# Performance work log

Measured on AMD Instinct MI355X. Metric: run time of the kernel, lower is better.

## Reference

```python
import jax, jax.numpy as jnp
import numpy as np
from jax import lax

B, T, D, LD, K = 128, 1024, 256, 512, 128
RD = LD + K  # 640 residual-LSTM width
PAD = 15     # (31 - 1) // 2 'same' padding for the LSA location conv


def _gru(x, h, wih, whh, bih, bhh):
    # torch.nn.GRUCell semantics, gate order [r, z, n]
    gi = x @ wih.T + bih
    gh = h @ whh.T + bhh
    ir, iz, inn = jnp.split(gi, 3, axis=-1)
    hr, hz, hn = jnp.split(gh, 3, axis=-1)
    r = jax.nn.sigmoid(ir + hr)
    z = jax.nn.sigmoid(iz + hz)
    n = jnp.tanh(inn + r * hn)
    return (1.0 - z) * n + z * h


def _lstm(x, h, c, wih, whh, bih, bhh):
    # torch.nn.LSTMCell semantics, gate order [i, f, g, o]
    g = x @ wih.T + bih + h @ whh.T + bhh
    i, f, gg, o = jnp.split(g, 4, axis=-1)
    c2 = jax.nn.sigmoid(f) * c + jax.nn.sigmoid(i) * jnp.tanh(gg)
    h2 = jax.nn.sigmoid(o) * jnp.tanh(c2)
    return h2, c2


def _forward(encoder_seq, encoder_seq_proj, prenet_in, attn_hidden, rnn1_h, rnn1_c,
             rnn2_h, rnn2_c, res_h, res_c, context_vec, cumulative, attn_prev,
             fc1_w, fc1_b, fc2_w, fc2_b, gru_wih, gru_whh, gru_bih, gru_bhh,
             conv_w, L_w, L_b, W_w, W_b, v_w, ri_w, ri_b,
             r1_wih, r1_whh, r1_bih, r1_bhh, r2_wih, r2_whh, r2_bih, r2_bhh,
             res_wih, res_whh, res_bih, res_bhh, stop_w, stop_b):
    # PreNet (dropout p = 0 in Decoder.__init__, so pure tanh-MLP)
    p = jnp.tanh(prenet_in @ fc1_w.T + fc1_b)
    prenet_out = jnp.tanh(p @ fc2_w.T + fc2_b)                     # [B, D//2]
    # Attention GRU
    attn_in = jnp.concatenate([context_vec, prenet_out], axis=-1)  # [B, D + D//2]
    attn_h = _gru(attn_in, attn_hidden, gru_wih, gru_whh, gru_bih, gru_bhh)  # [B, D]
    # LSA location-sensitive attention (cumulative/attn_prev are zeros at t=0)
    pq = (attn_h @ W_w.T + W_b)[:, None, :]                        # [B, 1, D]
    loc = jnp.stack([cumulative, attn_prev], axis=1)               # [B, 2, T]
    conv_out = lax.conv_general_dilated(loc, conv_w, (1,), [(PAD, PAD)],
                                        dimension_numbers=('NCH', 'OIH', 'NCH'))  # [B, 32, T]
    ploc = jnp.swapaxes(conv_out, 1, 2) @ L_w.T + L_b              # [B, T, D]
    u = jnp.squeeze(jnp.tanh(pq + encoder_seq_proj + ploc) @ v_w.T, -1)  # [B, T]
    sig = jax.nn.sigmoid(u)
    scores = sig / jnp.sum(sig, axis=1, keepdims=True)             # [B, T]
    cum_new = cumulative + scores
    context = jnp.einsum('bt,btd->bd', scores, encoder_seq)        # [B, D]
    # rnn_input projection + two residual LSTM cells (eval: no zoneout)
    x = jnp.concatenate([context, attn_h], axis=1) @ ri_w.T + ri_b  # [B, LD]
    h1, c1 = _lstm(x, rnn1_h, rnn1_c, r1_wih, r1_whh, r1_bih, r1_bhh)
    x = x + h1
    h2, c2 = _lstm(x, rnn2_h, rnn2_c, r2_wih, r2_whh, r2_bih, r2_bhh)
    x = x + h2
    # 4-layer residual LSTM stack on [prenet_in, x]
    res_x = jnp.concatenate([prenet_in, x], axis=1)                # [B, RD]
    hs, cs = [], []
    for i in range(4):
        hi, ci = _lstm(res_x, res_h[i], res_c[i], res_wih[i], res_whh[i], res_bih[i], res_bhh[i])
        res_x = res_x + hi
        hs.append(hi)
        cs.append(ci)
    cond = res_x                                                   # cond_features [B, RD]
    stop = jax.nn.sigmoid(cond @ stop_w.T + stop_b)                # [B, 1]
    return (cond, stop, scores, attn_h, h1, c1, h2, c2,
            jnp.stack(hs), jnp.stack(cs), context, cum_new)


def setup_inputs() -> dict:
    keys = iter(jax.random.split(jax.random.key(0), 64))
    nxt = lambda: next(keys)
    rn = lambda s: jax.random.normal(nxt(), s, jnp.float32)
    wp = lambda s: rn(s) * 0.02
    return {
        'encoder_seq': rn((B, T, D)),
        'encoder_seq_proj': rn((B, T, D)),
        'prenet_in': rn((B, K)),
        'attn_hidden': rn((B, D)),
        'rnn1_h': rn((B, LD)), 'rnn1_c': rn((B, LD)),
        'rnn2_h': rn((B, LD)), 'rnn2_c': rn((B, LD)),
        'res_h': rn((4, B, RD)), 'res_c': rn((4, B, RD)),
        'context_vec': rn((B, D)),
        'cumulative': jnp.zeros((B, T), jnp.float32),
        'attn_prev': jnp.zeros((B, T), jnp.float32),
        'fc1_w': wp((256, K)), 'fc1_b': jnp.zeros((256,), jnp.float32),
        'fc2_w': wp((D // 2, 256)), 'fc2_b': jnp.zeros((D // 2,), jnp.float32),
        'gru_wih': wp((3 * D, D + D // 2)), 'gru_whh': wp((3 * D, D)),
        'gru_bih': jnp.zeros((3 * D,), jnp.float32), 'gru_bhh': jnp.zeros((3 * D,), jnp.float32),
        'conv_w': wp((32, 2, 31)),
        'L_w': wp((D, 32)), 'L_b': jnp.zeros((D,), jnp.float32),
        'W_w': wp((D, D)), 'W_b': jnp.zeros((D,), jnp.float32),
        'v_w': wp((1, D)),
        'ri_w': wp((LD, 2 * D)), 'ri_b': jnp.zeros((LD,), jnp.float32),
        'r1_wih': wp((4 * LD, LD)), 'r1_whh': wp((4 * LD, LD)),
        'r1_bih': jnp.zeros((4 * LD,), jnp.float32), 'r1_bhh': jnp.zeros((4 * LD,), jnp.float32),
        'r2_wih': wp((4 * LD, LD)), 'r2_whh': wp((4 * LD, LD)),
        'r2_bih': jnp.zeros((4 * LD,), jnp.float32), 'r2_bhh': jnp.zeros((4 * LD,), jnp.float32),
        'res_wih': wp((4, 4 * RD, RD)), 'res_whh': wp((4, 4 * RD, RD)),
        'res_bih': jnp.zeros((4, 4 * RD), jnp.float32), 'res_bhh': jnp.zeros((4, 4 * RD), jnp.float32),
        'stop_w': wp((1, RD)), 'stop_b': jnp.zeros((1,), jnp.float32),
    }


def reference(encoder_seq, encoder_seq_proj, prenet_in, attn_hidden, rnn1_h, rnn1_c,
              rnn2_h, rnn2_c, res_h, res_c, context_vec, cumulative, attn_prev,
              fc1_w, fc1_b, fc2_w, fc2_b, gru_wih, gru_whh, gru_bih, gru_bhh,
              conv_w, L_w, L_b, W_w, W_b, v_w, ri_w, ri_b,
              r1_wih, r1_whh, r1_bih, r1_bhh, r2_wih, r2_whh, r2_bih, r2_bhh,
              res_wih, res_whh, res_bih, res_bhh, stop_w, stop_b):
    return _forward(encoder_seq, encoder_seq_proj, prenet_in, attn_hidden, rnn1_h, rnn1_c,
                    rnn2_h, rnn2_c, res_h, res_c, context_vec, cumulative, attn_prev,
                    fc1_w, fc1_b, fc2_w, fc2_b, gru_wih, gru_whh, gru_bih, gru_bhh,
                    conv_w, L_w, L_b, W_w, W_b, v_w, ri_w, ri_b,
                    r1_wih, r1_whh, r1_bih, r1_bhh, r2_wih, r2_whh, r2_bih, r2_bhh,
                    res_wih, res_whh, res_bih, res_bhh, stop_w, stop_b)
```

## Files before the change

### kernel.cpp

```cpp
#include <hip/hip_runtime.h>

#define DEV __device__ __forceinline__

DEV float sigm(float x) { return 1.0f / (1.0f + __expf(-x)); }
DEV float tanhf_fast(float x) { return 1.0f - 2.0f / (1.0f + __expf(2.0f * x)); }

__global__ __launch_bounds__(256) void gemm2s_kernel(
    const float* __restrict__ A1, int K1, const float* __restrict__ W1, int ldw1,
    const float* __restrict__ A2, int K2, const float* __restrict__ W2, int ldw2,
    float* __restrict__ Cp, int N, int KS, int KC)
{
    __shared__ float As[16][128];
    __shared__ float Ws[16][33];
    const int tid = threadIdx.x;
    const int chunk = blockIdx.x % KS;
    const int n0 = (blockIdx.x / KS) * 32;
    const int kbeg = chunk * KC;
    const int kend = kbeg + KC;
    const int tx = tid & 15, ty = tid >> 4;
    const int lm = tid & 127, lk = (tid >> 7) * 8;

    float acc[16];
#pragma unroll
    for (int i = 0; i < 16; ++i) acc[i] = 0.f;

    for (int k0 = kbeg; k0 < kend; k0 += 16) {
        const float* A; const float* W; int lda, ldw, kc;
        if (k0 < K1) { A = A1; W = W1; lda = K1; ldw = ldw1; kc = k0; }
        else         { A = A2; W = W2; lda = K2; ldw = ldw2; kc = k0 - K1; }

        float4 a0 = *(const float4*)(A + (size_t)lm * lda + kc + lk);
        float4 a1 = *(const float4*)(A + (size_t)lm * lda + kc + lk + 4);
        As[lk + 0][lm] = a0.x; As[lk + 1][lm] = a0.y;
        As[lk + 2][lm] = a0.z; As[lk + 3][lm] = a0.w;
        As[lk + 4][lm] = a1.x; As[lk + 5][lm] = a1.y;
        As[lk + 6][lm] = a1.z; As[lk + 7][lm] = a1.w;
        if (tid < 128) {
            int nl = tid >> 2, kq = (tid & 3) * 4;
            float4 w = *(const float4*)(W + (size_t)(n0 + nl) * ldw + kc + kq);
            Ws[kq + 0][nl] = w.x; Ws[kq + 1][nl] = w.y;
            Ws[kq + 2][nl] = w.z; Ws[kq + 3][nl] = w.w;
        }
        __syncthreads();
#pragma unroll
        for (int kk = 0; kk < 16; ++kk) {
            float w0 = Ws[kk][tx * 2 + 0];
            float w1 = Ws[kk][tx * 2 + 1];
            float4 x0 = *(const float4*)&As[kk][ty * 8];
            float4 x1 = *(const float4*)&As[kk][ty * 8 + 4];
            acc[0] += x0.x * w0; acc[1] += x0.y * w0;
            acc[2] += x0.z * w0; acc[3] += x0.w * w0;
            acc[4] += x1.x * w0; acc[5] += x1.y * w0;
            acc[6] += x1.z * w0; acc[7] += x1.w * w0;
            acc[8]  += x0.x * w1; acc[9]  += x0.y * w1;
            acc[10] += x0.z * w1; acc[11] += x0.w * w1;
            acc[12] += x1.x * w1; acc[13] += x1.y * w1;
            acc[14] += x1.z * w1; acc[15] += x1.w * w1;
        }
        __syncthreads();
    }

    float* Co = Cp + (size_t)chunk * 128 * N;
#pragma unroll
    for (int j = 0; j < 2; ++j) {
        int n = n0 + tx * 2 + j;
#pragma unroll
        for (int i = 0; i < 8; ++i)
            Co[(size_t)(ty * 8 + i) * N + n] = acc[j * 8 + i];
    }
}

__global__ void reduce_act_kernel(const float* __restrict__ p, int KS, int MN,
                                  const float* __restrict__ b,
                                  float* __restrict__ out, int N, int act)
{
    int idx = blockIdx.x * 256 + threadIdx.x;
    if (idx >= MN) return;
    int n = idx % N;
    float v = b ? b[n] : 0.f;
    for (int s = 0; s < KS; ++s) v += p[(size_t)s * MN + idx];
    if (act) v = tanhf_fast(v);
    out[idx] = v;
}

__global__ void gru_gate_kernel(const float* __restrict__ gi_p, int KSi,
                                const float* __restrict__ gh_p, int KSh,
                                const float* __restrict__ bih, const float* __restrict__ bhh,
                                const float* __restrict__ h, float* __restrict__ out)
{
    const size_t MN = 128 * 768;
    int m = blockIdx.x, d = threadIdx.x;
    size_t base = (size_t)m * 768 + d;
    float ir = bih[d], iz = bih[256 + d], in = bih[512 + d];
    for (int s = 0; s < KSi; ++s) {
        const float* p = gi_p + s * MN + base;
        ir += p[0]; iz += p[256]; in += p[512];
    }
    float hr = bhh[d], hz = bhh[256 + d], hn = bhh[512 + d];
    for (int s = 0; s < KSh; ++s) {
        const float* p = gh_p + s * MN + base;
        hr += p[0]; hz += p[256]; hn += p[512];
    }
    float r = sigm(ir + hr);
    float z = sigm(iz + hz);
    float n = tanhf_fast(in + r * hn);
    out[m * 256 + d] = (1.f - z) * n + z * h[m * 256 + d];
}

__global__ void lstm_gate_kernel(const float* __restrict__ gp, int KS,
                                 const float* __restrict__ bih, const float* __restrict__ bhh,
                                 const float* __restrict__ c_in,
                                 float* __restrict__ h_out, float* __restrict__ c_out,
                                 float* __restrict__ xacc, int H)
{
    int d = blockIdx.x * 256 + threadIdx.x;
    int m = blockIdx.y;
    if (d >= H) return;
    const size_t MN = (size_t)128 * 4 * H;
    size_t base = (size_t)m * 4 * H + d;
    float iv = bih[d] + bhh[d];
    float fv = bih[H + d] + bhh[H + d];
    float gv = bih[2 * H + d] + bhh[2 * H + d];
    float ov = bih[3 * H + d] + bhh[3 * H + d];
    for (int s = 0; s < KS; ++s) {
        const float* p = gp + s * MN + base;
        iv += p[0]; fv += p[H]; gv += p[2 * H]; ov += p[3 * H];
    }
    float c2 = sigm(fv) * c_in[m * H + d] + sigm(iv) * tanhf_fast(gv);
    float h2 = sigm(ov) * tanhf_fast(c2);
    h_out[m * H + d] = h2;
    c_out[m * H + d] = c2;
    if (xacc) xacc[m * H + d] += h2;
}

__global__ void transpose_lw_kernel(const float* __restrict__ Lw, float* __restrict__ LwT)
{
    int i = blockIdx.x * 256 + threadIdx.x;
    int c = i >> 8, d = i & 255;
    LwT[i] = Lw[d * 32 + c];
}

__global__ __launch_bounds__(256) void attn_u_kernel(
    const float* __restrict__ esp, const float* __restrict__ pq,
    const float* __restrict__ LwT, const float* __restrict__ Lb,
    const float* __restrict__ vw, const float* __restrict__ cw,
    const float* __restrict__ cum, const float* __restrict__ prev,
    float* __restrict__ sig_out)
{
    const int b = blockIdx.x >> 4;
    const int t0 = (blockIdx.x & 15) << 6;
    const int tid = threadIdx.x;

    __shared__ float cum_s[96], prev_s[96];
    __shared__ float cw_s[2][32][33];
    __shared__ float conv_s[32][68];
    __shared__ float Lw_s[32][256];
    __shared__ float pq_s[256], vw_s[256];

    if (tid < 94) {
        int ti = t0 - 15 + tid;
        cum_s[tid] = (ti >= 0 && ti < 1024) ? cum[b * 1024 + ti] : 0.f;
    } else if (tid >= 128 && tid < 222) {
        int i = tid - 128;
        int ti = t0 - 15 + i;
        prev_s[i] = (ti >= 0 && ti < 1024) ? prev[b * 1024 + ti] : 0.f;
    }
    for (int i = tid; i < 2048; i += 256) {
        int which = i >> 10, c = (i >> 5) & 31, k = i & 31;
        cw_s[which][c][k] = (k < 31) ? cw[(c * 2 + which) * 31 + k] : 0.f;
    }
    for (int i = tid; i < 8192; i += 256)
        (&Lw_s[0][0])[i] = LwT[i];
    pq_s[tid] = pq[b * 256 + tid] + Lb[tid];
    vw_s[tid] = vw[tid];
    __syncthreads();

    {
        int c = tid & 31, t8 = (tid >> 5) << 3;
        float a[8] = {0.f, 0.f, 0.f, 0.f, 0.f, 0.f, 0.f, 0.f};
        for (int k = 0; k < 31; ++k) {
            float w0 = cw_s[0][c][k], w1 = cw_s[1][c][k];
#pragma unroll
            for (int j = 0; j < 8; ++j)
                a[j] += w0 * cum_s[t8 + j + k] + w1 * prev_s[t8 + j + k];
        }
#pragma unroll
        for (int j = 0; j < 8; ++j) conv_s[c][t8 + j] = a[j];
    }
    __syncthreads();

    const int dg = (tid & 31) << 3;
    const int tg = (tid >> 5) << 3;
    float pl[8][8] = {};
#pragma unroll 4
    for (int c = 0; c < 32; ++c) {
        float4 lw0 = *(const float4*)&Lw_s[c][dg];
        float4 lw1 = *(const float4*)&Lw_s[c][dg + 4];
        float4 cv0 = *(const float4*)&conv_s[c][tg];
        float4 cv1 = *(const float4*)&conv_s[c][tg + 4];
        float lwv[8] = {lw0.x, lw0.y, lw0.z, lw0.w, lw1.x, lw1.y, lw1.z, lw1.w};
        float cvv[8] = {cv0.x, cv0.y, cv0.z, cv0.w, cv1.x, cv1.y, cv1.z, cv1.w};
#pragma unroll
        for (int jt = 0; jt < 8; ++jt)
#pragma unroll
            for (int jd = 0; jd < 8; ++jd)
                pl[jt][jd] += cvv[jt] * lwv[jd];
    }

    float4 pa = *(const float4*)&pq_s[dg];
    float4 pb = *(const float4*)&pq_s[dg + 4];
    float4 va = *(const float4*)&vw_s[dg];
    float4 vb = *(const float4*)&vw_s[dg + 4];
    float pqv[8] = {pa.x, pa.y, pa.z, pa.w, pb.x, pb.y, pb.z, pb.w};
    float vwv[8] = {va.x, va.y, va.z, va.w, vb.x, vb.y, vb.z, vb.w};

    float part[8];
#pragma unroll
    for (int jt = 0; jt < 8; ++jt) {
        int t = t0 + tg + jt;
        const float* er = esp + ((long)(b * 1024 + t) << 8) + dg;
        float4 e0 = *(const float4*)er;
        float4 e1 = *(const float4*)(er + 4);
        float ev[8] = {e0.x, e0.y, e0.z, e0.w, e1.x, e1.y, e1.z, e1.w};
        float s = 0.f;
#pragma unroll
        for (int jd = 0; jd < 8; ++jd)
            s += tanhf_fast(pqv[jd] + ev[jd] + pl[jt][jd]) * vwv[jd];
        part[jt] = s;
    }
#pragma unroll
    for (int off = 1; off < 32; off <<= 1)
#pragma unroll
        for (int jt = 0; jt < 8; ++jt)
            part[jt] += __shfl_xor(part[jt], off);
    if ((tid & 31) == 0) {
#pragma unroll
        for (int jt = 0; jt < 8; ++jt)
            sig_out[b * 1024 + t0 + tg + jt] = sigm(part[jt]);
    }
}

__global__ void attn_norm_kernel(const float* __restrict__ sig, const float* __restrict__ cum,
                                 float* __restrict__ scores, float* __restrict__ cum_new,
                                 float* __restrict__ ctx)
{
    __shared__ float red[4];
    int b = blockIdx.x, tid = threadIdx.x;
    float4 sv = *(const float4*)&sig[b * 1024 + tid * 4];
    float s = sv.x + sv.y + sv.z + sv.w;
#pragma unroll
    for (int off = 1; off < 64; off <<= 1) s += __shfl_xor(s, off);
    if ((tid & 63) == 0) red[tid >> 6] = s;
    __syncthreads();
    float inv = 1.f / (red[0] + red[1] + red[2] + red[3]);
    float4 cv = *(const float4*)&cum[b * 1024 + tid * 4];
    float4 sc = {sv.x * inv, sv.y * inv, sv.z * inv, sv.w * inv};
    *(float4*)&scores[b * 1024 + tid * 4] = sc;
    float4 cn = {cv.x + sc.x, cv.y + sc.y, cv.z + sc.z, cv.w + sc.w};
    *(float4*)&cum_new[b * 1024 + tid * 4] = cn;
    ctx[b * 256 + tid] = 0.f;
}

__global__ void attn_ctx_kernel(const float* __restrict__ scores, const float* __restrict__ es,
                                float* __restrict__ ctx)
{
    __shared__ float sc_s[256];
    int b = blockIdx.x >> 2;
    int tbase = (blockIdx.x & 3) * 256;
    int tid = threadIdx.x;
    sc_s[tid] = scores[b * 1024 + tbase + tid];
    __syncthreads();
    float a = 0.f;
    const float* ep = es + ((size_t)(b * 1024 + tbase)) * 256 + tid;
#pragma unroll 4
    for (int tt = 0; tt < 256; ++tt)
        a += sc_s[tt] * ep[(size_t)tt * 256];
    atomicAdd(&ctx[b * 256 + tid], a);
}

__global__ void build_rescat_kernel(const float* __restrict__ pre, const float* __restrict__ x,
                                    float* __restrict__ res)
{
    int idx = blockIdx.x * 256 + threadIdx.x;
    int m = idx / 640, d = idx - m * 640;
    res[idx] = (d < 128) ? pre[m * 128 + d] : x[m * 512 + d - 128];
}

__global__ void copy_kernel(const float* __restrict__ src, float* __restrict__ dst, int n)
{
    int idx = blockIdx.x * 256 + threadIdx.x;
    if (idx < n) dst[idx] = src[idx];
}

__global__ void stop_kernel(const float* __restrict__ res, const float* __restrict__ sw,
                            const float* __restrict__ sb, float* __restrict__ stop)
{
    int m = blockIdx.x, lane = threadIdx.x;
    float s = 0.f;
    for (int k = lane; k < 640; k += 64) s += res[m * 640 + k] * sw[k];
#pragma unroll
    for (int off = 1; off < 64; off <<= 1) s += __shfl_xor(s, off);
    if (lane == 0) stop[m] = sigm(s + sb[0]);
}

extern "C" void kernel_launch(void* const* d_in, const int* in_sizes, int n_in,
                              void* d_out, int out_size, void* d_ws, size_t ws_size,
                              hipStream_t stream)
{
    const float* encoder_seq      = (const float*)d_in[0];
    const float* encoder_seq_proj = (const float*)d_in[1];
    const float* prenet_in        = (const float*)d_in[2];
    const float* attn_hidden      = (const float*)d_in[3];
    const float* rnn1_h  = (const float*)d_in[4];
    const float* rnn1_c  = (const float*)d_in[5];
    const float* rnn2_h  = (const float*)d_in[6];
    const float* rnn2_c  = (const float*)d_in[7];
    const float* res_h   = (const float*)d_in[8];
    const float* res_c   = (const float*)d_in[9];
    const float* context_vec = (const float*)d_in[10];
    const float* cumulative  = (const float*)d_in[11];
    const float* attn_prev   = (const float*)d_in[12];
    const float* fc1_w = (const float*)d_in[13];
    const float* fc1_b = (const float*)d_in[14];
    const float* fc2_w = (const float*)d_in[15];
    const float* fc2_b = (const float*)d_in[16];
    const float* gru_wih = (const float*)d_in[17];
    const float* gru_whh = (const float*)d_in[18];
    const float* gru_bih = (const float*)d_in[19];
    const float* gru_bhh = (const float*)d_in[20];
    const float* conv_w = (const float*)d_in[21];
    const float* L_w = (const float*)d_in[22];
    const float* L_b = (const float*)d_in[23];
    const float* W_w = (const float*)d_in[24];
    const float* W_b = (const float*)d_in[25];
    const float* v_w = (const float*)d_in[26];
    const float* ri_w = (const float*)d_in[27];
    const float* ri_b = (const float*)d_in[28];
    const float* r1_wih = (const float*)d_in[29];
    const float* r1_whh = (const float*)d_in[30];
    const float* r1_bih = (const float*)d_in[31];
    const float* r1_bhh = (const float*)d_in[32];
    const float* r2_wih = (const float*)d_in[33];
    const float* r2_whh = (const float*)d_in[34];
    const float* r2_bih = (const float*)d_in[35];
    const float* r2_bhh = (const float*)d_in[36];
    const float* res_wih = (const float*)d_in[37];
    const float* res_whh = (const float*)d_in[38];
    const float* res_bih = (const float*)d_in[39];
    const float* res_bhh = (const float*)d_in[40];
    const float* stop_w = (const float*)d_in[41];
    const float* stop_b = (const float*)d_in[42];

    float* ws  = (float*)d_ws;
    float* out = (float*)d_out;

    const size_t OFF_P    = 0;
    const size_t OFF_POUT = 32768;
    const size_t OFF_PQ   = 49152;
    const size_t OFF_SIG  = 81920;
    const size_t OFF_X    = 212992;
    const size_t OFF_RES  = 278528;
    const size_t OFF_LWT  = 360448;
    const size_t OFF_PART = 368640;
    const size_t OFF_PARTB = OFF_PART + (size_t)8 * 128 * 768;

    const size_t O_COND   = 0;
    const size_t O_STOP   = 81920;
    const size_t O_SCORES = 82048;
    const size_t O_ATTNH  = 213120;
    const size_t O_H1     = 245888;
    const size_t O_C1     = 311424;
    const size_t O_H2     = 376960;
    const size_t O_C2     = 442496;
    const size_t O_HS     = 508032;
    const size_t O_CS     = 835712;
    const size_t O_CTX    = 1163392;
    const size_t O_CUM    = 1196160;

    transpose_lw_kernel<<<32, 256, 0, stream>>>(L_w, ws + OFF_LWT);

    gemm2s_kernel<<<8 * 4, 256, 0, stream>>>(prenet_in, 128, fc1_w, 128,
                                             nullptr, 0, nullptr, 0,
                                             ws + OFF_PART, 256, 4, 32);
    reduce_act_kernel<<<128, 256, 0, stream>>>(ws + OFF_PART, 4, 128 * 256, fc1_b,
                                               ws + OFF_P, 256, 1);
    gemm2s_kernel<<<4 * 8, 256, 0, stream>>>(ws + OFF_P, 256, fc2_w, 256,
                                             nullptr, 0, nullptr, 0,
                                             ws + OFF_PART, 128, 8, 32);
    reduce_act_kernel<<<64, 256, 0, stream>>>(ws + OFF_PART, 8, 128 * 128, fc2_b,
                                              ws + OFF_POUT, 128, 1);

    gemm2s_kernel<<<24 * 8, 256, 0, stream>>>(context_vec, 256, gru_wih, 384,
                                              ws + OFF_POUT, 128, gru_wih + 256, 384,
                                              ws + OFF_PART, 768, 8, 48);
    gemm2s_kernel<<<24 * 8, 256, 0, stream>>>(attn_hidden, 256, gru_whh, 256,
                                              nullptr, 0, nullptr, 0,
                                              ws + OFF_PARTB, 768, 8, 32);
    gru_gate_kernel<<<128, 256, 0, stream>>>(ws + OFF_PART, 8, ws + OFF_PARTB, 8,
                                             gru_bih, gru_bhh, attn_hidden, out + O_ATTNH);

    gemm2s_kernel<<<8 * 8, 256, 0, stream>>>(out + O_ATTNH, 256, W_w, 256,
                                             nullptr, 0, nullptr, 0,
                                             ws + OFF_PART, 256, 8, 32);
    reduce_act_kernel<<<128, 256, 0, stream>>>(ws + OFF_PART, 8, 128 * 256, W_b,
                                               ws + OFF_PQ, 256, 0);

    attn_u_kernel<<<2048, 256, 0, stream>>>(encoder_seq_proj, ws + OFF_PQ, ws + OFF_LWT,
                                            L_b, v_w, conv_w, cumulative, attn_prev,
                                            ws + OFF_SIG);
    attn_norm_kernel<<<128, 256, 0, stream>>>(ws + OFF_SIG, cumulative,
                                              out + O_SCORES, out + O_CUM, out + O_CTX);
    attn_ctx_kernel<<<512, 256, 0, stream>>>(out + O_SCORES, encoder_seq, out + O_CTX);

    gemm2s_kernel<<<16 * 8, 256, 0, stream>>>(out + O_CTX, 256, ri_w, 512,
                                              out + O_ATTNH, 256, ri_w + 256, 512,
                                              ws + OFF_PART, 512, 8, 64);
    reduce_act_kernel<<<256, 256, 0, stream>>>(ws + OFF_PART, 8, 128 * 512, ri_b,
                                               ws + OFF_X, 512, 0);

    gemm2s_kernel<<<64 * 8, 256, 0, stream>>>(ws + OFF_X, 512, r1_wih, 512,
                                              rnn1_h, 512, r1_whh, 512,
                                              ws + OFF_PART, 2048, 8, 128);
    lstm_gate_kernel<<<dim3(2, 128), 256, 0, stream>>>(ws + OFF_PART, 8, r1_bih, r1_bhh,
                                                       rnn1_c, out + O_H1, out + O_C1,
                                                       ws + OFF_X, 512);
    gemm2s_kernel<<<64 * 8, 256, 0, stream>>>(ws + OFF_X, 512, r2_wih, 512,
                                              rnn2_h, 512, r2_whh, 512,
                                              ws + OFF_PART, 2048, 8, 128);
    lstm_gate_kernel<<<dim3(2, 128), 256, 0, stream>>>(ws + OFF_PART, 8, r2_bih, r2_bhh,
                                                       rnn2_c, out + O_H2, out + O_C2,
                                                       ws + OFF_X, 512);

    build_rescat_kernel<<<320, 256, 0, stream>>>(prenet_in, ws + OFF_X, ws + OFF_RES);

    for (int i = 0; i < 4; ++i) {
        const float* wih = res_wih + (size_t)i * 2560 * 640;
        const float* whh = res_whh + (size_t)i * 2560 * 640;
        gemm2s_kernel<<<80 * 8, 256, 0, stream>>>(ws + OFF_RES, 640, wih, 640,
                                                  res_h + (size_t)i * 81920, 640, whh, 640,
                                                  ws + OFF_PART, 2560, 8, 160);
        lstm_gate_kernel<<<dim3(3, 128), 256, 0, stream>>>(ws + OFF_PART, 8,
                                                           res_bih + (size_t)i * 2560,
                                                           res_bhh + (size_t)i * 2560,
                                                           res_c + (size_t)i * 81920,
                                                           out + O_HS + (size_t)i * 81920,
                                                           out + O_CS + (size_t)i * 81920,
                                                           ws + OFF_RES, 640);
    }

    copy_kernel<<<320, 256, 0, stream>>>(ws + OFF_RES, out + O_COND, 128 * 640);
    stop_kernel<<<128, 64, 0, stream>>>(ws + OFF_RES, stop_w, stop_b, out + O_STOP);
}
```

Baseline: 672.4 us.

## Use bf16 MFMA for location projection, double-buffer GEMM, split context kernel

The location-feature projection inside the attention-energy kernel now runs as a bf16 16x16x32 MFMA. The conv output and L_w are rounded to bf16 in shared memory, replacing the fp32 outer-product loop. The split-K GEMM gains register-staged double buffering so global loads for the next tile overlap compute on the current one. The context kernel is split into twice as many blocks over shorter time chunks, and sigmoid/tanh/normalisation use hardware reciprocal. The bf16 rounding and approximate reciprocal reduce precision.

```diff
diff --git a/kernel.cpp b/kernel.cpp
--- a/kernel.cpp
+++ b/kernel.cpp
@@ -2,21 +2,31 @@
 
 #define DEV __device__ __forceinline__
 
-DEV float sigm(float x) { return 1.0f / (1.0f + __expf(-x)); }
-DEV float tanhf_fast(float x) { return 1.0f - 2.0f / (1.0f + __expf(2.0f * x)); }
+typedef __attribute__((ext_vector_type(8))) short short8;
+typedef __attribute__((ext_vector_type(4))) float f32x4;
+
+DEV float fast_rcp(float x) { return __builtin_amdgcn_rcpf(x); }
+DEV float sigm(float x) { return fast_rcp(1.0f + __expf(-x)); }
+DEV float tanhf_fast(float x) { return 1.0f - 2.0f * fast_rcp(1.0f + __expf(2.0f * x)); }
+
+DEV short f2bf(float f) {
+    unsigned u = __float_as_uint(f);
+    unsigned r = (u + 0x7FFFu + ((u >> 16) & 1u)) >> 16;
+    return (short)r;
+}
 
 __global__ __launch_bounds__(256) void gemm2s_kernel(
     const float* __restrict__ A1, int K1, const float* __restrict__ W1, int ldw1,
     const float* __restrict__ A2, int K2, const float* __restrict__ W2, int ldw2,
     float* __restrict__ Cp, int N, int KS, int KC)
 {
-    __shared__ float As[16][128];
-    __shared__ float Ws[16][33];
+    __shared__ float As[2][16][128];
+    __shared__ float Ws[2][16][33];
     const int tid = threadIdx.x;
     const int chunk = blockIdx.x % KS;
     const int n0 = (blockIdx.x / KS) * 32;
     const int kbeg = chunk * KC;
-    const int kend = kbeg + KC;
+    const int nt = KC / 16;
     const int tx = tid & 15, ty = tid >> 4;
     const int lm = tid & 127, lk = (tid >> 7) * 8;
 
@@ -24,30 +34,43 @@
 #pragma unroll
     for (int i = 0; i < 16; ++i) acc[i] = 0.f;
 
-    for (int k0 = kbeg; k0 < kend; k0 += 16) {
+    float4 ra0, ra1, rw;
+    auto load_regs = [&](int k0) {
         const float* A; const float* W; int lda, ldw, kc;
         if (k0 < K1) { A = A1; W = W1; lda = K1; ldw = ldw1; kc = k0; }
         else         { A = A2; W = W2; lda = K2; ldw = ldw2; kc = k0 - K1; }
-
-        float4 a0 = *(const float4*)(A + (size_t)lm * lda + kc + lk);
-        float4 a1 = *(const float4*)(A + (size_t)lm * lda + kc + lk + 4);
-        As[lk + 0][lm] = a0.x; As[lk + 1][lm] = a0.y;
-        As[lk + 2][lm] = a0.z; As[lk + 3][lm] = a0.w;
-        As[lk + 4][lm] = a1.x; As[lk + 5][lm] = a1.y;
-        As[lk + 6][lm] = a1.z; As[lk + 7][lm] = a1.w;
+        ra0 = *(const float4*)(A + (size_t)lm * lda + kc + lk);
+        ra1 = *(const float4*)(A + (size_t)lm * lda + kc + lk + 4);
         if (tid < 128) {
             int nl = tid >> 2, kq = (tid & 3) * 4;
-            float4 w = *(const float4*)(W + (size_t)(n0 + nl) * ldw + kc + kq);
-            Ws[kq + 0][nl] = w.x; Ws[kq + 1][nl] = w.y;
-            Ws[kq + 2][nl] = w.z; Ws[kq + 3][nl] = w.w;
+            rw = *(const float4*)(W + (size_t)(n0 + nl) * ldw + kc + kq);
         }
-        __syncthreads();
+    };
+    auto store_lds = [&](int buf) {
+        As[buf][lk + 0][lm] = ra0.x; As[buf][lk + 1][lm] = ra0.y;
+        As[buf][lk + 2][lm] = ra0.z; As[buf][lk + 3][lm] = ra0.w;
+        As[buf][lk + 4][lm] = ra1.x; As[buf][lk + 5][lm] = ra1.y;
+        As[buf][lk + 6][lm] = ra1.z; As[buf][lk + 7][lm] = ra1.w;
+        if (tid < 128) {
+            int nl = tid >> 2, kq = (tid & 3) * 4;
+            Ws[buf][kq + 0][nl] = rw.x; Ws[buf][kq + 1][nl] = rw.y;
+            Ws[buf][kq + 2][nl] = rw.z; Ws[buf][kq + 3][nl] = rw.w;
+        }
+    };
+
+    load_regs(kbeg);
+    store_lds(0);
+    __syncthreads();
+
+    for (int it = 0; it < nt; ++it) {
+        const int cur = it & 1;
+        if (it + 1 < nt) load_regs(kbeg + (it + 1) * 16);
 #pragma unroll
         for (int kk = 0; kk < 16; ++kk) {
-            float w0 = Ws[kk][tx * 2 + 0];
-            float w1 = Ws[kk][tx * 2 + 1];
-            float4 x0 = *(const float4*)&As[kk][ty * 8];
-            float4 x1 = *(const float4*)&As[kk][ty * 8 + 4];
+            float w0 = Ws[cur][kk][tx * 2 + 0];
+            float w1 = Ws[cur][kk][tx * 2 + 1];
+            float4 x0 = *(const float4*)&As[cur][kk][ty * 8];
+            float4 x1 = *(const float4*)&As[cur][kk][ty * 8 + 4];
             acc[0] += x0.x * w0; acc[1] += x0.y * w0;
             acc[2] += x0.z * w0; acc[3] += x0.w * w0;
             acc[4] += x1.x * w0; acc[5] += x1.y * w0;
@@ -57,6 +80,7 @@
             acc[12] += x1.x * w1; acc[13] += x1.y * w1;
             acc[14] += x1.z * w1; acc[15] += x1.w * w1;
         }
+        if (it + 1 < nt) store_lds(cur ^ 1);
         __syncthreads();
     }
 
@@ -133,16 +157,15 @@
     if (xacc) xacc[m * H + d] += h2;
 }
 
-__global__ void transpose_lw_kernel(const float* __restrict__ Lw, float* __restrict__ LwT)
+__global__ void lw_bf16_kernel(const float* __restrict__ Lw, short* __restrict__ LwBf)
 {
     int i = blockIdx.x * 256 + threadIdx.x;
-    int c = i >> 8, d = i & 255;
-    LwT[i] = Lw[d * 32 + c];
+    LwBf[i] = f2bf(Lw[i]);
 }
 
 __global__ __launch_bounds__(256) void attn_u_kernel(
     const float* __restrict__ esp, const float* __restrict__ pq,
-    const float* __restrict__ LwT, const float* __restrict__ Lb,
+    const short* __restrict__ LwBf, const float* __restrict__ Lb,
     const float* __restrict__ vw, const float* __restrict__ cw,
     const float* __restrict__ cum, const float* __restrict__ prev,
     float* __restrict__ sig_out)
@@ -151,10 +174,10 @@
     const int t0 = (blockIdx.x & 15) << 6;
     const int tid = threadIdx.x;
 
-    __shared__ float cum_s[96], prev_s[96];
+    __shared__ float cum_s[94], prev_s[94];
     __shared__ float cw_s[2][32][33];
-    __shared__ float conv_s[32][68];
-    __shared__ float Lw_s[32][256];
+    __shared__ short conv_bf[64 * 32];
+    __shared__ short lw_bf[256 * 32];
     __shared__ float pq_s[256], vw_s[256];
 
     if (tid < 94) {
@@ -169,8 +192,12 @@
         int which = i >> 10, c = (i >> 5) & 31, k = i & 31;
         cw_s[which][c][k] = (k < 31) ? cw[(c * 2 + which) * 31 + k] : 0.f;
     }
-    for (int i = tid; i < 8192; i += 256)
-        (&Lw_s[0][0])[i] = LwT[i];
+    {
+        const int4* src = (const int4*)LwBf;
+        int4* dst = (int4*)lw_bf;
+#pragma unroll
+        for (int k = 0; k < 4; ++k) dst[tid + k * 256] = src[tid + k * 256];
+    }
     pq_s[tid] = pq[b * 256 + tid] + Lb[tid];
     vw_s[tid] = vw[tid];
     __syncthreads();
@@ -185,59 +212,36 @@
                 a[j] += w0 * cum_s[t8 + j + k] + w1 * prev_s[t8 + j + k];
         }
 #pragma unroll
-        for (int j = 0; j < 8; ++j) conv_s[c][t8 + j] = a[j];
+        for (int j = 0; j < 8; ++j) conv_bf[(t8 + j) * 32 + c] = f2bf(a[j]);
     }
     __syncthreads();
 
-    const int dg = (tid & 31) << 3;
-    const int tg = (tid >> 5) << 3;
-    float pl[8][8] = {};
-#pragma unroll 4
-    for (int c = 0; c < 32; ++c) {
-        float4 lw0 = *(const float4*)&Lw_s[c][dg];
-        float4 lw1 = *(const float4*)&Lw_s[c][dg + 4];
-        float4 cv0 = *(const float4*)&conv_s[c][tg];
-        float4 cv1 = *(const float4*)&conv_s[c][tg + 4];
-        float lwv[8] = {lw0.x, lw0.y, lw0.z, lw0.w, lw1.x, lw1.y, lw1.z, lw1.w};
-        float cvv[8] = {cv0.x, cv0.y, cv0.z, cv0.w, cv1.x, cv1.y, cv1.z, cv1.w};
-#pragma unroll
-        for (int jt = 0; jt < 8; ++jt)
-#pragma unroll
-            for (int jd = 0; jd < 8; ++jd)
-                pl[jt][jd] += cvv[jt] * lwv[jd];
-    }
-
-    float4 pa = *(const float4*)&pq_s[dg];
-    float4 pb = *(const float4*)&pq_s[dg + 4];
-    float4 va = *(const float4*)&vw_s[dg];
-    float4 vb = *(const float4*)&vw_s[dg + 4];
-    float pqv[8] = {pa.x, pa.y, pa.z, pa.w, pb.x, pb.y, pb.z, pb.w};
-    float vwv[8] = {va.x, va.y, va.z, va.w, vb.x, vb.y, vb.z, vb.w};
-
-    float part[8];
-#pragma unroll
-    for (int jt = 0; jt < 8; ++jt) {
-        int t = t0 + tg + jt;
-        const float* er = esp + ((long)(b * 1024 + t) << 8) + dg;
-        float4 e0 = *(const float4*)er;
-        float4 e1 = *(const float4*)(er + 4);
-        float ev[8] = {e0.x, e0.y, e0.z, e0.w, e1.x, e1.y, e1.z, e1.w};
-        float s = 0.f;
-#pragma unroll
-        for (int jd = 0; jd < 8; ++jd)
-            s += tanhf_fast(pqv[jd] + ev[jd] + pl[jt][jd]) * vwv[jd];
-        part[jt] = s;
-    }
-#pragma unroll
-    for (int off = 1; off < 32; off <<= 1)
-#pragma unroll
-        for (int jt = 0; jt < 8; ++jt)
-            part[jt] += __shfl_xor(part[jt], off);
-    if ((tid & 31) == 0) {
-#pragma unroll
-        for (int jt = 0; jt < 8; ++jt)
-            sig_out[b * 1024 + t0 + tg + jt] = sigm(part[jt]);
-    }
+    const int lane = tid & 63, w = tid >> 6;
+    const int q = lane >> 4, c16 = lane & 15;
+    const int myt = t0 + w * 16 + c16;
+
+    short8 bfrag = *(const short8*)&conv_bf[(w * 16 + c16) * 32 + q * 8];
+    const float* er = esp + ((size_t)(b * 1024 + myt) << 8);
+
+    float s = 0.f;
+#pragma unroll
+    for (int dt = 0; dt < 16; ++dt) {
+        short8 afrag = *(const short8*)&lw_bf[(dt * 16 + c16) * 32 + q * 8];
+        f32x4 acc = {0.f, 0.f, 0.f, 0.f};
+        acc = __builtin_amdgcn_mfma_f32_16x16x32_bf16(afrag, bfrag, acc, 0, 0, 0);
+        const int d0 = dt * 16 + q * 4;
+        float4 e   = *(const float4*)(er + d0);
+        float4 pqv = *(const float4*)&pq_s[d0];
+        float4 vwv = *(const float4*)&vw_s[d0];
+        s += tanhf_fast(pqv.x + e.x + acc[0]) * vwv.x;
+        s += tanhf_fast(pqv.y + e.y + acc[1]) * vwv.y;
+        s += tanhf_fast(pqv.z + e.z + acc[2]) * vwv.z;
+        s += tanhf_fast(pqv.w + e.w + acc[3]) * vwv.w;
+    }
+    s += __shfl_xor(s, 16);
+    s += __shfl_xor(s, 32);
+    if (lane < 16)
+        sig_out[b * 1024 + t0 + w * 16 + lane] = sigm(s);
 }
 
 __global__ void attn_norm_kernel(const float* __restrict__ sig, const float* __restrict__ cum,
@@ -252,7 +256,7 @@
     for (int off = 1; off < 64; off <<= 1) s += __shfl_xor(s, off);
     if ((tid & 63) == 0) red[tid >> 6] = s;
     __syncthreads();
-    float inv = 1.f / (red[0] + red[1] + red[2] + red[3]);
+    float inv = fast_rcp(red[0] + red[1] + red[2] + red[3]);
     float4 cv = *(const float4*)&cum[b * 1024 + tid * 4];
     float4 sc = {sv.x * inv, sv.y * inv, sv.z * inv, sv.w * inv};
     *(float4*)&scores[b * 1024 + tid * 4] = sc;
@@ -264,16 +268,16 @@
 __global__ void attn_ctx_kernel(const float* __restrict__ scores, const float* __restrict__ es,
                                 float* __restrict__ ctx)
 {
-    __shared__ float sc_s[256];
-    int b = blockIdx.x >> 2;
-    int tbase = (blockIdx.x & 3) * 256;
+    __shared__ float sc_s[128];
+    int b = blockIdx.x >> 3;
+    int tbase = (blockIdx.x & 7) * 128;
     int tid = threadIdx.x;
-    sc_s[tid] = scores[b * 1024 + tbase + tid];
+    if (tid < 128) sc_s[tid] = scores[b * 1024 + tbase + tid];
     __syncthreads();
     float a = 0.f;
     const float* ep = es + ((size_t)(b * 1024 + tbase)) * 256 + tid;
 #pragma unroll 4
-    for (int tt = 0; tt < 256; ++tt)
+    for (int tt = 0; tt < 128; ++tt)
         a += sc_s[tt] * ep[(size_t)tt * 256];
     atomicAdd(&ctx[b * 256 + tid], a);
 }
@@ -377,7 +381,8 @@
     const size_t O_CTX    = 1163392;
     const size_t O_CUM    = 1196160;
 
-    transpose_lw_kernel<<<32, 256, 0, stream>>>(L_w, ws + OFF_LWT);
+    short* lwbf = (short*)(ws + OFF_LWT);
+    lw_bf16_kernel<<<32, 256, 0, stream>>>(L_w, lwbf);
 
     gemm2s_kernel<<<8 * 4, 256, 0, stream>>>(prenet_in, 128, fc1_w, 128,
                                              nullptr, 0, nullptr, 0,
@@ -405,12 +410,12 @@
     reduce_act_kernel<<<128, 256, 0, stream>>>(ws + OFF_PART, 8, 128 * 256, W_b,
                                                ws + OFF_PQ, 256, 0);
 
-    attn_u_kernel<<<2048, 256, 0, stream>>>(encoder_seq_proj, ws + OFF_PQ, ws + OFF_LWT,
+    attn_u_kernel<<<2048, 256, 0, stream>>>(encoder_seq_proj, ws + OFF_PQ, lwbf,
                                             L_b, v_w, conv_w, cumulative, attn_prev,
                                             ws + OFF_SIG);
     attn_norm_kernel<<<128, 256, 0, stream>>>(ws + OFF_SIG, cumulative,
                                               out + O_SCORES, out + O_CUM, out + O_CTX);
-    attn_ctx_kernel<<<512, 256, 0, stream>>>(out + O_SCORES, encoder_seq, out + O_CTX);
+    attn_ctx_kernel<<<1024, 256, 0, stream>>>(out + O_SCORES, encoder_seq, out + O_CTX);
 
     gemm2s_kernel<<<16 * 8, 256, 0, stream>>>(out + O_CTX, 256, ri_w, 512,
                                               out + O_ATTNH, 256, ri_w + 256, 512,
```

Result: no change. 660.3 us (-1.8%).
